# Performance work log

Measured on AMD Instinct MI355X. Metric: run time of the kernel, lower is better.

Reference implementation:

```python
import jax, jax.numpy as jnp
import numpy as np

EPSILON = 1e-8
N, M, D = 8192, 8192, 128
NUM_LABELS = 10


def setup_inputs() -> dict:
    key = jax.random.key(0)
    k1, k2, k3 = jax.random.split(key, 3)
    a = jax.random.normal(k1, (N, D), dtype=jnp.float32)
    b = jax.random.normal(k2, (M, D), dtype=jnp.float32)
    labels_for_a = jax.random.randint(k3, (N,), 0, NUM_LABELS, dtype=jnp.int64)
    return {"a": a, "b": b, "labels_for_a": labels_for_a}


def reference(a, b, labels_for_a):
    d = a.shape[1]
    # p: [n, m] scaled similarity
    p = jnp.matmul(a, b.T) / jnp.sqrt(jnp.float32(d))
    ab = jax.nn.softmax(p, axis=1)        # [n, m] walk a->b
    ba = jax.nn.softmax(p.T, axis=1)      # [m, n] walk b->a
    aba = jnp.matmul(ab, ba)              # [n, n] round-trip probability
    # label-equality targets, normalized per row
    labels = labels_for_a[None, :]
    is_same_label = (labels == labels.T).astype(jnp.float32)  # [n, n]
    label_count = is_same_label.sum(axis=1, keepdims=True)
    targets = is_same_label / label_count
    walker_loss = -(targets * jnp.log(EPSILON + aba)).sum(axis=1).mean(axis=0)
    # visit loss: uniform target over b
    visit_probability = ab.mean(axis=0)   # [m]
    m = b.shape[0]
    uniform = jnp.float32(1.0 / m)
    visit_loss = -(uniform * jnp.log(EPSILON + visit_probability)).sum(axis=0)
    return (walker_loss, visit_loss)
```

## Files before the change

### kernel.cpp

```cpp
#include <hip/hip_runtime.h>


typedef __attribute__((ext_vector_type(8))) short bf16x8;
typedef __attribute__((ext_vector_type(4))) float f32x4;

#define NROW 8192
#define DIM 128
#define NLAB 10
#define EPSf 1e-8f
#define SF 0.35709582f
#define LAM 64.0f
#define ILAM2 (1.0f / 4096.0f)
#define SPLIT 4
#define NPAIR 36
#define SPSTRIDE (360 * 16384)
#define LROW 144

#define O_WA 0
#define O_VA 8
#define O_CNT 64
#define O_OFF 128
#define O_SIDX 256
#define O_PS 33280
#define O_CS 1081856
#define O_VK 1114624
#define O_CV 1147392
#define O_CKS 1180160
#define O_ABF 1212928
#define O_BBF 3310080
#define O_E 5407232
#define O_SP 72516096

__device__ __forceinline__ unsigned short f2bf(float f) {
  unsigned u = __builtin_bit_cast(unsigned, f);
  u += 0x7fffu + ((u >> 16) & 1u);
  return (unsigned short)(u >> 16);
}
__device__ __forceinline__ float bf2f(unsigned short s) {
  unsigned u = ((unsigned)s) << 16;
  return __builtin_bit_cast(float, u);
}
__device__ __forceinline__ unsigned char f2fp8(float f) {
  int v = __builtin_amdgcn_cvt_pk_fp8_f32(f, f, 0, false);
  return (unsigned char)(v & 0xff);
}

__global__ __launch_bounds__(256) void k_bucket(const int* __restrict__ lab,
                                                int* cnt, int* offs, int* sidx,
                                                double* wa, double* va,
                                                float* cs, float* vk) {
  __shared__ int lc[NLAB], lcur[NLAB];
  int tid = threadIdx.x;
  if (tid < NLAB) lc[tid] = 0;
  __syncthreads();
  for (int i = tid; i < NROW; i += 256) {
    int l = lab[i]; l = l < 0 ? 0 : (l > 9 ? 9 : l);
    atomicAdd(&lc[l], 1);
  }
  for (int i = tid; i < NROW; i += 256) { cs[i] = 0.f; vk[i] = 0.f; }
  __syncthreads();
  if (tid == 0) {
    int run = 0;
    for (int l = 0; l < NLAB; ++l) { cnt[l] = lc[l]; offs[l] = run; lcur[l] = run; run += lc[l]; }
    *wa = 0.0; *va = 0.0;
  }
  __syncthreads();
  for (int i = tid; i < NROW; i += 256) {
    int l = lab[i]; l = l < 0 ? 0 : (l > 9 ? 9 : l);
    int p = atomicAdd(&lcur[l], 1);
    sidx[p] = i;
  }
}

__global__ __launch_bounds__(256) void k_convert(const float* __restrict__ X,
                                                 unsigned short* __restrict__ Y) {
  int i = (blockIdx.x * 256 + threadIdx.x) * 8;
  f32x4 a = *(const f32x4*)(X + i);
  f32x4 b = *(const f32x4*)(X + i + 4);
  bf16x8 o;
  o[0] = (short)f2bf(a[0] * SF); o[1] = (short)f2bf(a[1] * SF);
  o[2] = (short)f2bf(a[2] * SF); o[3] = (short)f2bf(a[3] * SF);
  o[4] = (short)f2bf(b[0] * SF); o[5] = (short)f2bf(b[1] * SF);
  o[6] = (short)f2bf(b[2] * SF); o[7] = (short)f2bf(b[3] * SF);
  *(bf16x8*)(Y + i) = o;
}

__global__ __launch_bounds__(256, 2) void k_stats(const unsigned short* __restrict__ Abf,
                                                  const unsigned short* __restrict__ Bbf,
                                                  const int* __restrict__ sidx,
                                                  float* __restrict__ ps,
                                                  float* __restrict__ CS) {
  __shared__ int gidx[128];
  int tid = threadIdx.x;
  if (tid < 128) gidx[tid] = sidx[blockIdx.x * 128 + tid];
  __syncthreads();
  int wave = tid >> 6, lane = tid & 63;
  int wrow = wave >> 1, wcol = wave & 1;
  int m = lane & 15, quad = lane >> 4;
  bf16x8 af[4][4];
#pragma unroll
  for (int mi = 0; mi < 4; ++mi) {
    int gi = gidx[wrow * 64 + mi * 16 + m];
#pragma unroll
    for (int ks = 0; ks < 4; ++ks)
      af[mi][ks] = *(const bf16x8*)(Abf + gi * DIM + ks * 32 + quad * 8);
  }
  float tsum[4][4];
#pragma unroll
  for (int mi = 0; mi < 4; ++mi)
#pragma unroll
    for (int r = 0; r < 4; ++r) tsum[mi][r] = 0.f;
  int p0 = blockIdx.x * 128 + wrow * 64;
  for (int t = 0; t < 4; ++t) {
    int c0 = blockIdx.y * 512 + t * 128 + wcol * 64;
    bf16x8 bfr[4][4];
#pragma unroll
    for (int ni = 0; ni < 4; ++ni)
#pragma unroll
      for (int ks = 0; ks < 4; ++ks)
        bfr[ni][ks] = *(const bf16x8*)(Bbf + (c0 + ni * 16 + m) * DIM + ks * 32 + quad * 8);
    f32x4 acc[4][4];
#pragma unroll
    for (int mi = 0; mi < 4; ++mi)
#pragma unroll
      for (int ni = 0; ni < 4; ++ni) acc[mi][ni] = (f32x4){0.f, 0.f, 0.f, 0.f};
#pragma unroll
    for (int ks = 0; ks < 4; ++ks)
#pragma unroll
      for (int mi = 0; mi < 4; ++mi)
#pragma unroll
        for (int ni = 0; ni < 4; ++ni)
          acc[mi][ni] = __builtin_amdgcn_mfma_f32_16x16x32_bf16(af[mi][ks], bfr[ni][ks], acc[mi][ni], 0, 0, 0);
    float csum[4] = {0.f, 0.f, 0.f, 0.f};
#pragma unroll
    for (int mi = 0; mi < 4; ++mi)
#pragma unroll
      for (int ni = 0; ni < 4; ++ni)
#pragma unroll
        for (int r = 0; r < 4; ++r) {
          float e = __builtin_amdgcn_exp2f(acc[mi][ni][r]);
          tsum[mi][r] += e;
          csum[ni] += e;
        }
#pragma unroll
    for (int ni = 0; ni < 4; ++ni) {
      csum[ni] += __shfl_xor(csum[ni], 16);
      csum[ni] += __shfl_xor(csum[ni], 32);
    }
    if (lane < 16) {
#pragma unroll
      for (int ni = 0; ni < 4; ++ni) atomicAdd(&CS[c0 + ni * 16 + lane], csum[ni]);
    }
  }
#pragma unroll
  for (int off = 1; off < 16; off <<= 1)
#pragma unroll
    for (int mi = 0; mi < 4; ++mi)
#pragma unroll
      for (int r = 0; r < 4; ++r) tsum[mi][r] += __shfl_xor(tsum[mi][r], off);
  if (m == 0) {
#pragma unroll
    for (int mi = 0; mi < 4; ++mi)
#pragma unroll
      for (int r = 0; r < 4; ++r)
        ps[(blockIdx.y * 2 + wcol) * NROW + p0 + mi * 16 + quad * 4 + r] = tsum[mi][r];
  }
}

__global__ __launch_bounds__(256) void k_mstats(const float* __restrict__ ps,
                                                const float* __restrict__ CS,
                                                float* __restrict__ CVs,
                                                float* __restrict__ CKS) {
  int i = blockIdx.x * 256 + threadIdx.x;
  float s = 0.f;
#pragma unroll
  for (int t = 0; t < 32; ++t) s += ps[t * NROW + i];
  CVs[i] = 1.f / s;
  CKS[i] = rsqrtf(CS[i]);
}

__global__ __launch_bounds__(256, 2) void k_fill(const unsigned short* __restrict__ Abf,
                                                 const unsigned short* __restrict__ Bbf,
                                                 const int* __restrict__ sidx,
                                                 const float* __restrict__ CVs,
                                                 const float* __restrict__ CKS,
                                                 unsigned char* __restrict__ E,
                                                 float* __restrict__ VK) {
  __shared__ int gidx[128];
  int tid = threadIdx.x;
  if (tid < 128) gidx[tid] = sidx[blockIdx.x * 128 + tid];
  __syncthreads();
  int wave = tid >> 6, lane = tid & 63;
  int wrow = wave >> 1, wcol = wave & 1;
  int m = lane & 15, quad = lane >> 4;
  int p0 = blockIdx.x * 128 + wrow * 64;
  bf16x8 af[4][4];
  float cv16[4][4];
#pragma unroll
  for (int mi = 0; mi < 4; ++mi) {
    int gi = gidx[wrow * 64 + mi * 16 + m];
#pragma unroll
    for (int ks = 0; ks < 4; ++ks)
      af[mi][ks] = *(const bf16x8*)(Abf + gi * DIM + ks * 32 + quad * 8);
#pragma unroll
    for (int r = 0; r < 4; ++r) cv16[mi][r] = CVs[p0 + mi * 16 + quad * 4 + r];
  }
  for (int t = 0; t < 4; ++t) {
    int c0 = blockIdx.y * 512 + t * 128 + wcol * 64;
    bf16x8 bfr[4][4];
    float ck4[4];
#pragma unroll
    for (int ni = 0; ni < 4; ++ni) {
      ck4[ni] = CKS[c0 + ni * 16 + m] * LAM;
#pragma unroll
      for (int ks = 0; ks < 4; ++ks)
        bfr[ni][ks] = *(const bf16x8*)(Bbf + (c0 + ni * 16 + m) * DIM + ks * 32 + quad * 8);
    }
    f32x4 acc[4][4];
#pragma unroll
    for (int mi = 0; mi < 4; ++mi)
#pragma unroll
      for (int ni = 0; ni < 4; ++ni) acc[mi][ni] = (f32x4){0.f, 0.f, 0.f, 0.f};
#pragma unroll
    for (int ks = 0; ks < 4; ++ks)
#pragma unroll
      for (int mi = 0; mi < 4; ++mi)
#pragma unroll
        for (int ni = 0; ni < 4; ++ni)
          acc[mi][ni] = __builtin_amdgcn_mfma_f32_16x16x32_bf16(af[mi][ks], bfr[ni][ks], acc[mi][ni], 0, 0, 0);
    float csum[4] = {0.f, 0.f, 0.f, 0.f};
#pragma unroll
    for (int mi = 0; mi < 4; ++mi)
#pragma unroll
      for (int ni = 0; ni < 4; ++ni)
#pragma unroll
        for (int r = 0; r < 4; ++r) {
          float e = __builtin_amdgcn_exp2f(acc[mi][ni][r]);
          int row = p0 + mi * 16 + quad * 4 + r;
          E[(size_t)row * NROW + c0 + ni * 16 + m] = f2fp8(e * ck4[ni]);
          csum[ni] = fmaf(e, cv16[mi][r], csum[ni]);
        }
#pragma unroll
    for (int ni = 0; ni < 4; ++ni) {
      csum[ni] += __shfl_xor(csum[ni], 16);
      csum[ni] += __shfl_xor(csum[ni], 32);
    }
    if (lane < 16) {
#pragma unroll
      for (int ni = 0; ni < 4; ++ni) atomicAdd(&VK[c0 + ni * 16 + lane], csum[ni]);
    }
  }
}

__global__ __launch_bounds__(256) void k_vloss(const float* __restrict__ VK, double* va) {
  __shared__ float red[4];
  int tid = threadIdx.x;
  int i = blockIdx.x * 256 + tid;
  float l = __logf(EPSf + VK[i] * (1.f / 8192.f));
#pragma unroll
  for (int off = 32; off; off >>= 1) l += __shfl_down(l, off);
  if ((tid & 63) == 0) red[tid >> 6] = l;
  __syncthreads();
  if (tid == 0) {
    double tot = (double)red[0] + (double)red[1] + (double)red[2] + (double)red[3];
    atomicAdd(va, -tot / 8192.0);
  }
}

__global__ __launch_bounds__(256, 4) void k_gram(const unsigned char* __restrict__ Eh,
                                                 const int* __restrict__ cnt,
                                                 const int* __restrict__ offs,
                                                 unsigned short* __restrict__ Spart) {
  int gid = blockIdx.x;
  int xcd = gid & 7, slot = gid >> 3;
  int group = xcd * 5 + slot / NPAIR;
  int pidx = slot % NPAIR;
  int lab = group / SPLIT, split = group % SPLIT;
  int tj = 0;
  while ((tj + 1) * (tj + 2) / 2 <= pidx) ++tj;
  int ti = pidx - tj * (tj + 1) / 2;
  int c = cnt[lab], o = offs[lab];
  if (tj * 128 >= c) return;
  const bool diag = (ti == tj);
  __shared__ __align__(16) unsigned char Pt[128 * LROW];
  __shared__ __align__(16) unsigned char Rt[128 * LROW];
  int tid = threadIdx.x;
  int wave = tid >> 6, lane = tid & 63;
  int wrow = wave >> 1, wcol = wave & 1;
  int m = lane & 15, quad = lane >> 4;
  const unsigned char* pp[4];
  const unsigned char* pr[4];
  int lo[4];
#pragma unroll
  for (int v = 0; v < 4; ++v) {
    int slotv = v * 256 + tid, row = slotv >> 3, c8 = slotv & 7;
    int ri = o + ti * 128 + row; if (ri > NROW - 1) ri = NROW - 1;
    int rj = o + tj * 128 + row; if (rj > NROW - 1) rj = NROW - 1;
    pp[v] = Eh + (size_t)ri * NROW + split * 2048 + c8 * 8;
    pr[v] = Eh + (size_t)rj * NROW + split * 2048 + c8 * 8;
    lo[v] = row * LROW + c8 * 8;
  }
  f32x4 acc[4][4];
#pragma unroll
  for (int mi = 0; mi < 4; ++mi)
#pragma unroll
    for (int ni = 0; ni < 4; ++ni) acc[mi][ni] = (f32x4){0.f, 0.f, 0.f, 0.f};
  const unsigned char* Bt = diag ? Pt : Rt;
  for (int t = 0; t < 32; ++t) {
    __syncthreads();
    unsigned long dp[4], dr[4];
#pragma unroll
    for (int v = 0; v < 4; ++v) {
      dp[v] = *(const unsigned long*)(pp[v]); pp[v] += 64;
      if (!diag) { dr[v] = *(const unsigned long*)(pr[v]); pr[v] += 64; }
    }
#pragma unroll
    for (int v = 0; v < 4; ++v) {
      *(unsigned long*)(Pt + lo[v]) = dp[v];
      if (!diag) *(unsigned long*)(Rt + lo[v]) = dr[v];
    }
    __syncthreads();
#pragma unroll
    for (int ks = 0; ks < 2; ++ks) {
      long pa[4], rb[4];
#pragma unroll
      for (int mi = 0; mi < 4; ++mi) {
        int row = wrow * 64 + mi * 16 + m;
        pa[mi] = *(const long*)(Pt + row * LROW + (ks * 4 + quad) * 8);
      }
#pragma unroll
      for (int ni = 0; ni < 4; ++ni) {
        int row = wcol * 64 + ni * 16 + m;
        rb[ni] = *(const long*)(Bt + row * LROW + (ks * 4 + quad) * 8);
      }
#pragma unroll
      for (int mi = 0; mi < 4; ++mi)
#pragma unroll
        for (int ni = 0; ni < 4; ++ni)
          acc[mi][ni] = __builtin_amdgcn_mfma_f32_16x16x32_fp8_fp8(pa[mi], rb[ni], acc[mi][ni], 0, 0, 0);
    }
  }
  size_t base = (size_t)(split * SPSTRIDE) + (size_t)(lab * NPAIR + pidx) * 16384;
#pragma unroll
  for (int mi = 0; mi < 4; ++mi)
#pragma unroll
    for (int ni = 0; ni < 4; ++ni) {
      ushort4 w4;
      w4.x = f2bf(acc[mi][ni][0]);
      w4.y = f2bf(acc[mi][ni][1]);
      w4.z = f2bf(acc[mi][ni][2]);
      w4.w = f2bf(acc[mi][ni][3]);
      *(ushort4*)(Spart + base + (size_t)(mi * 4 + ni) * 1024 + tid * 4) = w4;
    }
}

__global__ __launch_bounds__(256) void k_reduce(const unsigned short* __restrict__ Spart,
                                                const int* __restrict__ cnt,
                                                const int* __restrict__ offs,
                                                const float* __restrict__ CVs,
                                                double* wa) {
  int lab = blockIdx.y, pidx = blockIdx.x;
  int tj = 0;
  while ((tj + 1) * (tj + 2) / 2 <= pidx) ++tj;
  int ti = pidx - tj * (tj + 1) / 2;
  int c = cnt[lab], o = offs[lab];
  if (tj * 128 >= c) return;
  __shared__ float isei[128], isej[128];
  __shared__ float red[4];
  int tid = threadIdx.x;
  if (tid < 128) {
    int ri = o + ti * 128 + tid; if (ri > NROW - 1) ri = NROW - 1;
    int rj = o + tj * 128 + tid; if (rj > NROW - 1) rj = NROW - 1;
    isei[tid] = CVs[ri] * ILAM2;
    isej[tid] = CVs[rj] * ILAM2;
  }
  __syncthreads();
  int wave = tid >> 6, lane = tid & 63;
  int wrow = wave >> 1, wcol = wave & 1;
  int m = lane & 15, quad = lane >> 4;
  size_t base = (size_t)(lab * NPAIR + pidx) * 16384;
  float lsum = 0.f;
#pragma unroll
  for (int mi = 0; mi < 4; ++mi)
#pragma unroll
    for (int ni = 0; ni < 4; ++ni) {
      size_t off = base + (size_t)(mi * 4 + ni) * 1024 + tid * 4;
      ushort4 s0 = *(const ushort4*)(Spart + off);
      ushort4 s1 = *(const ushort4*)(Spart + SPSTRIDE + off);
      ushort4 s2 = *(const ushort4*)(Spart + 2 * (size_t)SPSTRIDE + off);
      ushort4 s3 = *(const ushort4*)(Spart + 3 * (size_t)SPSTRIDE + off);
      float S[4];
      S[0] = bf2f(s0.x) + bf2f(s1.x) + bf2f(s2.x) + bf2f(s3.x);
      S[1] = bf2f(s0.y) + bf2f(s1.y) + bf2f(s2.y) + bf2f(s3.y);
      S[2] = bf2f(s0.z) + bf2f(s1.z) + bf2f(s2.z) + bf2f(s3.z);
      S[3] = bf2f(s0.w) + bf2f(s1.w) + bf2f(s2.w) + bf2f(s3.w);
      int jl = wcol * 64 + ni * 16 + m;
      int j = tj * 128 + jl;
#pragma unroll
      for (int r = 0; r < 4; ++r) {
        int il = wrow * 64 + mi * 16 + quad * 4 + r;
        int i = ti * 128 + il;
        if (i < c && j < c) {
          lsum += __logf(EPSf + S[r] * isei[il]);
          if (ti != tj) lsum += __logf(EPSf + S[r] * isej[jl]);
        }
      }
    }
#pragma unroll
  for (int off2 = 32; off2; off2 >>= 1) lsum += __shfl_down(lsum, off2);
  if (lane == 0) red[wave] = lsum;
  __syncthreads();
  if (tid == 0) {
    double tot = (double)red[0] + (double)red[1] + (double)red[2] + (double)red[3];
    atomicAdd(wa, -tot / (8192.0 * (double)c));
  }
}

__global__ void k_finish(const double* wa, const double* va, float* out) {
  out[0] = (float)(*wa);
  out[1] = (float)(*va);
}

extern "C" void kernel_launch(void* const* d_in, const int* in_sizes, int n_in,
                              void* d_out, int out_size, void* d_ws, size_t ws_size,
                              hipStream_t stream) {
  const float* A = (const float*)d_in[0];
  const float* B = (const float*)d_in[1];
  const int* LAB = (const int*)d_in[2];
  float* out = (float*)d_out;
  char* w = (char*)d_ws;
  double* WA = (double*)(w + O_WA);
  double* VA = (double*)(w + O_VA);
  int* CNT = (int*)(w + O_CNT);
  int* OFFS = (int*)(w + O_OFF);
  int* SIDX = (int*)(w + O_SIDX);
  float* PS = (float*)(w + O_PS);
  float* CS = (float*)(w + O_CS);
  float* VK = (float*)(w + O_VK);
  float* CVs = (float*)(w + O_CV);
  float* CKS = (float*)(w + O_CKS);
  unsigned short* ABF = (unsigned short*)(w + O_ABF);
  unsigned short* BBF = (unsigned short*)(w + O_BBF);
  unsigned char* E = (unsigned char*)(w + O_E);
  unsigned short* SP = (unsigned short*)(w + O_SP);

  k_bucket<<<1, 256, 0, stream>>>(LAB, CNT, OFFS, SIDX, WA, VA, CS, VK);
  k_convert<<<512, 256, 0, stream>>>(A, ABF);
  k_convert<<<512, 256, 0, stream>>>(B, BBF);
  k_stats<<<dim3(64, 16), 256, 0, stream>>>(ABF, BBF, SIDX, PS, CS);
  k_mstats<<<32, 256, 0, stream>>>(PS, CS, CVs, CKS);
  k_fill<<<dim3(64, 16), 256, 0, stream>>>(ABF, BBF, SIDX, CVs, CKS, E, VK);
  k_vloss<<<32, 256, 0, stream>>>(VK, VA);
  k_gram<<<NPAIR * SPLIT * NLAB, 256, 0, stream>>>(E, CNT, OFFS, SP);
  k_reduce<<<dim3(NPAIR, NLAB), 256, 0, stream>>>(SP, CNT, OFFS, CVs, WA);
  k_finish<<<1, 1, 0, stream>>>(WA, VA, out);
}
```

Baseline: 285.8 us.

## Stream GEMM fragments per k-step, raise occupancy, interleave fp8 LDS tile for wide reads

k_stats and k_fill no longer hold the whole A/B bf16 fragment sets in registers; they load A and B fragments per k-step inside the MFMA loop, and launch bounds are raised to three blocks per SIMD-group. The fp8 pair-GEMM kernel shrinks its LDS row pitch and interleaves the 8-byte chunks so each lane reads both k-steps with one 16-byte LDS load. The aim is fewer VGPRs for more occupancy and fewer LDS instructions. In exchange A fragments are reloaded for every column tile, and the new LDS layout may change bank-conflict behaviour.

After: 400.2 us. 40.0% more time.

```diff
diff --git a/kernel.cpp b/kernel.cpp
--- a/kernel.cpp
+++ b/kernel.cpp
@@ -3,6 +3,7 @@
 
 typedef __attribute__((ext_vector_type(8))) short bf16x8;
 typedef __attribute__((ext_vector_type(4))) float f32x4;
+typedef __attribute__((ext_vector_type(2))) long longx2;
 
 #define NROW 8192
 #define DIM 128
@@ -14,7 +15,7 @@
 #define SPLIT 4
 #define NPAIR 36
 #define SPSTRIDE (360 * 16384)
-#define LROW 144
+#define LROW 80
 
 #define O_WA 0
 #define O_VA 8
@@ -85,7 +86,7 @@
   *(bf16x8*)(Y + i) = o;
 }
 
-__global__ __launch_bounds__(256, 2) void k_stats(const unsigned short* __restrict__ Abf,
+__global__ __launch_bounds__(256, 3) void k_stats(const unsigned short* __restrict__ Abf,
                                                   const unsigned short* __restrict__ Bbf,
                                                   const int* __restrict__ sidx,
                                                   float* __restrict__ ps,
@@ -97,14 +98,9 @@
   int wave = tid >> 6, lane = tid & 63;
   int wrow = wave >> 1, wcol = wave & 1;
   int m = lane & 15, quad = lane >> 4;
-  bf16x8 af[4][4];
-#pragma unroll
-  for (int mi = 0; mi < 4; ++mi) {
-    int gi = gidx[wrow * 64 + mi * 16 + m];
-#pragma unroll
-    for (int ks = 0; ks < 4; ++ks)
-      af[mi][ks] = *(const bf16x8*)(Abf + gi * DIM + ks * 32 + quad * 8);
-  }
+  int gi[4];
+#pragma unroll
+  for (int mi = 0; mi < 4; ++mi) gi[mi] = gidx[wrow * 64 + mi * 16 + m];
   float tsum[4][4];
 #pragma unroll
   for (int mi = 0; mi < 4; ++mi)
@@ -113,24 +109,26 @@
   int p0 = blockIdx.x * 128 + wrow * 64;
   for (int t = 0; t < 4; ++t) {
     int c0 = blockIdx.y * 512 + t * 128 + wcol * 64;
-    bf16x8 bfr[4][4];
-#pragma unroll
-    for (int ni = 0; ni < 4; ++ni)
-#pragma unroll
-      for (int ks = 0; ks < 4; ++ks)
-        bfr[ni][ks] = *(const bf16x8*)(Bbf + (c0 + ni * 16 + m) * DIM + ks * 32 + quad * 8);
     f32x4 acc[4][4];
 #pragma unroll
     for (int mi = 0; mi < 4; ++mi)
 #pragma unroll
       for (int ni = 0; ni < 4; ++ni) acc[mi][ni] = (f32x4){0.f, 0.f, 0.f, 0.f};
 #pragma unroll
-    for (int ks = 0; ks < 4; ++ks)
+    for (int ks = 0; ks < 4; ++ks) {
+      bf16x8 af[4], bfr[4];
 #pragma unroll
       for (int mi = 0; mi < 4; ++mi)
+        af[mi] = *(const bf16x8*)(Abf + gi[mi] * DIM + ks * 32 + quad * 8);
+#pragma unroll
+      for (int ni = 0; ni < 4; ++ni)
+        bfr[ni] = *(const bf16x8*)(Bbf + (c0 + ni * 16 + m) * DIM + ks * 32 + quad * 8);
+#pragma unroll
+      for (int mi = 0; mi < 4; ++mi)
 #pragma unroll
         for (int ni = 0; ni < 4; ++ni)
-          acc[mi][ni] = __builtin_amdgcn_mfma_f32_16x16x32_bf16(af[mi][ks], bfr[ni][ks], acc[mi][ni], 0, 0, 0);
+          acc[mi][ni] = __builtin_amdgcn_mfma_f32_16x16x32_bf16(af[mi], bfr[ni], acc[mi][ni], 0, 0, 0);
+    }
     float csum[4] = {0.f, 0.f, 0.f, 0.f};
 #pragma unroll
     for (int mi = 0; mi < 4; ++mi)
@@ -179,7 +177,7 @@
   CKS[i] = rsqrtf(CS[i]);
 }
 
-__global__ __launch_bounds__(256, 2) void k_fill(const unsigned short* __restrict__ Abf,
+__global__ __launch_bounds__(256, 3) void k_fill(const unsigned short* __restrict__ Abf,
                                                  const unsigned short* __restrict__ Bbf,
                                                  const int* __restrict__ sidx,
                                                  const float* __restrict__ CVs,
@@ -194,40 +192,39 @@
   int wrow = wave >> 1, wcol = wave & 1;
   int m = lane & 15, quad = lane >> 4;
   int p0 = blockIdx.x * 128 + wrow * 64;
-  bf16x8 af[4][4];
+  int gi[4];
   float cv16[4][4];
 #pragma unroll
   for (int mi = 0; mi < 4; ++mi) {
-    int gi = gidx[wrow * 64 + mi * 16 + m];
-#pragma unroll
-    for (int ks = 0; ks < 4; ++ks)
-      af[mi][ks] = *(const bf16x8*)(Abf + gi * DIM + ks * 32 + quad * 8);
+    gi[mi] = gidx[wrow * 64 + mi * 16 + m];
 #pragma unroll
     for (int r = 0; r < 4; ++r) cv16[mi][r] = CVs[p0 + mi * 16 + quad * 4 + r];
   }
   for (int t = 0; t < 4; ++t) {
     int c0 = blockIdx.y * 512 + t * 128 + wcol * 64;
-    bf16x8 bfr[4][4];
     float ck4[4];
 #pragma unroll
-    for (int ni = 0; ni < 4; ++ni) {
-      ck4[ni] = CKS[c0 + ni * 16 + m] * LAM;
-#pragma unroll
-      for (int ks = 0; ks < 4; ++ks)
-        bfr[ni][ks] = *(const bf16x8*)(Bbf + (c0 + ni * 16 + m) * DIM + ks * 32 + quad * 8);
-    }
+    for (int ni = 0; ni < 4; ++ni) ck4[ni] = CKS[c0 + ni * 16 + m] * LAM;
     f32x4 acc[4][4];
 #pragma unroll
     for (int mi = 0; mi < 4; ++mi)
 #pragma unroll
       for (int ni = 0; ni < 4; ++ni) acc[mi][ni] = (f32x4){0.f, 0.f, 0.f, 0.f};
 #pragma unroll
-    for (int ks = 0; ks < 4; ++ks)
+    for (int ks = 0; ks < 4; ++ks) {
+      bf16x8 af[4], bfr[4];
 #pragma unroll
       for (int mi = 0; mi < 4; ++mi)
+        af[mi] = *(const bf16x8*)(Abf + gi[mi] * DIM + ks * 32 + quad * 8);
+#pragma unroll
+      for (int ni = 0; ni < 4; ++ni)
+        bfr[ni] = *(const bf16x8*)(Bbf + (c0 + ni * 16 + m) * DIM + ks * 32 + quad * 8);
+#pragma unroll
+      for (int mi = 0; mi < 4; ++mi)
 #pragma unroll
         for (int ni = 0; ni < 4; ++ni)
-          acc[mi][ni] = __builtin_amdgcn_mfma_f32_16x16x32_bf16(af[mi][ks], bfr[ni][ks], acc[mi][ni], 0, 0, 0);
+          acc[mi][ni] = __builtin_amdgcn_mfma_f32_16x16x32_bf16(af[mi], bfr[ni], acc[mi][ni], 0, 0, 0);
+    }
     float csum[4] = {0.f, 0.f, 0.f, 0.f};
 #pragma unroll
     for (int mi = 0; mi < 4; ++mi)
@@ -298,7 +295,8 @@
     int rj = o + tj * 128 + row; if (rj > NROW - 1) rj = NROW - 1;
     pp[v] = Eh + (size_t)ri * NROW + split * 2048 + c8 * 8;
     pr[v] = Eh + (size_t)rj * NROW + split * 2048 + c8 * 8;
-    lo[v] = row * LROW + c8 * 8;
+    int pos = (c8 & 3) * 2 + (c8 >> 2);
+    lo[v] = row * LROW + pos * 8;
   }
   f32x4 acc[4][4];
 #pragma unroll
@@ -320,25 +318,27 @@
       if (!diag) *(unsigned long*)(Rt + lo[v]) = dr[v];
     }
     __syncthreads();
-#pragma unroll
-    for (int ks = 0; ks < 2; ++ks) {
-      long pa[4], rb[4];
-#pragma unroll
-      for (int mi = 0; mi < 4; ++mi) {
-        int row = wrow * 64 + mi * 16 + m;
-        pa[mi] = *(const long*)(Pt + row * LROW + (ks * 4 + quad) * 8);
-      }
-#pragma unroll
-      for (int ni = 0; ni < 4; ++ni) {
-        int row = wcol * 64 + ni * 16 + m;
-        rb[ni] = *(const long*)(Bt + row * LROW + (ks * 4 + quad) * 8);
-      }
-#pragma unroll
-      for (int mi = 0; mi < 4; ++mi)
-#pragma unroll
-        for (int ni = 0; ni < 4; ++ni)
-          acc[mi][ni] = __builtin_amdgcn_mfma_f32_16x16x32_fp8_fp8(pa[mi], rb[ni], acc[mi][ni], 0, 0, 0);
-    }
+    longx2 pa[4], rb[4];
+#pragma unroll
+    for (int mi = 0; mi < 4; ++mi) {
+      int row = wrow * 64 + mi * 16 + m;
+      pa[mi] = *(const longx2*)(Pt + row * LROW + quad * 16);
+    }
+#pragma unroll
+    for (int ni = 0; ni < 4; ++ni) {
+      int row = wcol * 64 + ni * 16 + m;
+      rb[ni] = *(const longx2*)(Bt + row * LROW + quad * 16);
+    }
+#pragma unroll
+    for (int mi = 0; mi < 4; ++mi)
+#pragma unroll
+      for (int ni = 0; ni < 4; ++ni)
+        acc[mi][ni] = __builtin_amdgcn_mfma_f32_16x16x32_fp8_fp8(pa[mi][0], rb[ni][0], acc[mi][ni], 0, 0, 0);
+#pragma unroll
+    for (int mi = 0; mi < 4; ++mi)
+#pragma unroll
+      for (int ni = 0; ni < 4; ++ni)
+        acc[mi][ni] = __builtin_amdgcn_mfma_f32_16x16x32_fp8_fp8(pa[mi][1], rb[ni][1], acc[mi][ni], 0, 0, 0);
   }
   size_t base = (size_t)(split * SPSTRIDE) + (size_t)(lab * NPAIR + pidx) * 16384;
 #pragma unroll
```
